# Kernel optimization log

Hardware: AMD Instinct MI355X
Metric: run time of the kernel (lower is better)

## Reference

```python
import jax, jax.numpy as jnp
import numpy as np

B, I, H = 16384, 1024, 1024
W_SCALE = 0.03  # keep gate pre-activations in a sane range (mimics small init)


def setup_inputs() -> dict:
    key = jax.random.key(0)
    ks = jax.random.split(key, 7)
    return {
        "x": jax.random.normal(ks[0], (B, I), dtype=jnp.float32),
        "c": jax.random.normal(ks[1], (B, H), dtype=jnp.float32),
        "h": jax.random.normal(ks[2], (B, H), dtype=jnp.float32),
        # gate order along axis 0: f (forget), i (input), k (cell cand), o (output)
        "Wx": jax.random.normal(ks[3], (4, H, I), dtype=jnp.float32) * W_SCALE,
        "bx": jax.random.normal(ks[4], (4, H), dtype=jnp.float32) * W_SCALE,
        "Wh": jax.random.normal(ks[5], (4, H, H), dtype=jnp.float32) * W_SCALE,
        "bh": jax.random.normal(ks[6], (4, H), dtype=jnp.float32) * W_SCALE,
    }


def reference(x, c, h, Wx, bx, Wh, bh):
    # Fused equivalent of the 8 tiny nn.Linear calls: one stacked GEMM each
    # for input->hidden and hidden->hidden. pre: [B, 4, H]
    pre = (jnp.einsum('bi,ghi->bgh', x, Wx)
           + jnp.einsum('bk,ghk->bgh', h, Wh)
           + bx[None] + bh[None])
    f = jax.nn.sigmoid(pre[:, 0])   # forget gate (w1/r1)
    i = jax.nn.sigmoid(pre[:, 1])   # input gate  (w2/r2)
    k = jnp.tanh(pre[:, 2])         # cell candidate (w3/r3)
    o = jax.nn.sigmoid(pre[:, 3])   # output gate (w4/r4)
    c_new = f * c + i * k
    h_new = o * jnp.tanh(c_new)
    return (o, c_new, h_new)
```

## Files before the change

### kernel.cpp

```cpp
#include <hip/hip_runtime.h>
#include <hip/hip_bf16.h>
#include <cstdint>

#define DI __device__ __forceinline__

typedef __attribute__((ext_vector_type(4))) float f32x4;
typedef __attribute__((ext_vector_type(8))) short bf16x8;

static constexpr int B_ = 16384, I_ = 1024, H_ = 1024;
static constexpr int M = B_;
static constexpr int N = 4 * H_;
static constexpr int K = I_ + H_;
static constexpr int NT = K / 64;

static constexpr size_t OFF_A  = 0;
static constexpr size_t OFF_W  = OFF_A + (size_t)M * K * 2;
static constexpr size_t OFF_BI = OFF_W + (size_t)N * K * 2;
static constexpr size_t OFF_G  = OFF_BI + (size_t)N * 4;

DI unsigned short f2bf(float f) {
    union { float f; unsigned u; } v; v.f = f;
    unsigned r = v.u + 0x7FFFu + ((v.u >> 16) & 1u);
    return (unsigned short)(r >> 16);
}
DI float bf2f(unsigned short u) {
    union { unsigned u; float f; } v; v.u = ((unsigned)u) << 16; return v.f;
}

__global__ void cvt_kernel(const float* __restrict__ x, const float* __restrict__ h,
                           const float* __restrict__ Wx, const float* __restrict__ Wh,
                           unsigned short* __restrict__ A, unsigned short* __restrict__ W)
{
    long tid = (long)blockIdx.x * blockDim.x + threadIdx.x;
    long row = tid >> 9;
    int  col = (int)(tid & 511) * 4;
    const float* src;
    unsigned short* dst;
    if (row < M) {
        src = (col < I_) ? x + (size_t)row * I_ + col
                         : h + (size_t)row * H_ + (col - I_);
        dst = A + (size_t)row * K + col;
    } else {
        long r = row - M;
        src = (col < I_) ? Wx + (size_t)r * I_ + col
                         : Wh + (size_t)r * H_ + (col - I_);
        dst = W + (size_t)r * K + col;
    }
    float4 v = *(const float4*)src;
    ushort4 o;
    o.x = f2bf(v.x); o.y = f2bf(v.y); o.z = f2bf(v.z); o.w = f2bf(v.w);
    *(ushort4*)dst = o;
}

__global__ void bias_kernel(const float* __restrict__ bx, const float* __restrict__ bh,
                            float* __restrict__ bias)
{
    int i = blockIdx.x * blockDim.x + threadIdx.x;
    if (i < N) bias[i] = bx[i] + bh[i];
}

DI void stage_half(const unsigned short* __restrict__ g, int grow0, int kcol,
                   unsigned short* ldsbase, int tid)
{
    const int w    = tid >> 6, lane = tid & 63;
    const int rsub = (w << 3) + (lane >> 3);
    const int kk   = kcol + (((lane & 7) ^ (lane >> 3)) << 3);
#pragma unroll
    for (int l = 0; l < 2; ++l) {
        const unsigned short* gp = g + (size_t)(grow0 + (l << 6) + rsub) * K + kk;
        unsigned short* lp = ldsbase + (((l << 6) + (w << 3)) << 6);
        __builtin_amdgcn_global_load_lds(
            (const __attribute__((address_space(1))) void*)gp,
            (__attribute__((address_space(3))) void*)lp, 16, 0, 0);
    }
}

DI bf16x8 ldfrag(const unsigned short* tile, int row, int ks, int lane)
{
    const int sl = ((ks << 2) + (lane >> 4)) ^ (lane & 7);
    return *(const bf16x8*)(tile + (row << 6) + (sl << 3));
}

DI void fbar() {
    __builtin_amdgcn_sched_barrier(0);
    __builtin_amdgcn_s_barrier();
    __builtin_amdgcn_sched_barrier(0);
}

#define MFMA_QUAD(MH, N0)                                                     \
  _Pragma("unroll") for (int m_ = 0; m_ < 4; ++m_)                            \
  _Pragma("unroll") for (int dn_ = 0; dn_ < 2; ++dn_)                         \
  _Pragma("unroll") for (int ks_ = 0; ks_ < 2; ++ks_)                         \
    acc[(MH)*4 + m_][(N0) + dn_] = __builtin_amdgcn_mfma_f32_16x16x32_bf16(   \
        a[m_][ks_], b[(N0) + dn_][ks_], acc[(MH)*4 + m_][(N0) + dn_], 0, 0, 0);

__global__ __launch_bounds__(512, 2) void gemm_gates(
    const unsigned short* __restrict__ Abf, const unsigned short* __restrict__ Wbf,
    const float* __restrict__ bias, __hip_bfloat16* __restrict__ G)
{
    __shared__ __align__(16) unsigned short sh[65536];

    const int tid  = threadIdx.x;
    const int lane = tid & 63;
    const int wid  = tid >> 6;
    const int wr   = wid >> 2;
    const int wc   = wid & 3;

    const int bid  = blockIdx.x;
    const int wg   = ((bid & 7) << 7) | (bid >> 3);
    const int nbk  = wg & 15, mbk = wg >> 4;
    const int brow = mbk << 8, bcol = nbk << 8;

    const int l15  = lane & 15;
    const int rA0  = (wr << 7) + l15;
    const int rB0  = (wc << 6) + l15;

    f32x4 acc[8][4];
#pragma unroll
    for (int i = 0; i < 8; ++i)
#pragma unroll
        for (int j = 0; j < 4; ++j) acc[i][j] = f32x4{0.f, 0.f, 0.f, 0.f};
    bf16x8 a[4][2], b[4][2];

    {
        unsigned short* A0 = sh;
        unsigned short* B0 = sh + 16384;
        unsigned short* A1 = sh + 32768;
        stage_half(Abf, brow,       0, A0,        tid);
        stage_half(Abf, brow + 128, 0, A0 + 8192, tid);
        stage_half(Wbf, bcol,       0, B0,        tid);
        stage_half(Wbf, bcol + 128, 0, B0 + 8192, tid);
        stage_half(Abf, brow,      64, A1,        tid);
        asm volatile("s_waitcnt vmcnt(2)" ::: "memory");
        fbar();
    }

    for (int t = 0; t < NT; ++t) {
        const int q = t & 1;
        unsigned short* curA = sh + q * 32768;
        unsigned short* curB = curA + 16384;
        unsigned short* nxtA = sh + (q ^ 1) * 32768;
        unsigned short* nxtB = nxtA + 16384;
        const int k1 = (t + 1) << 6, k2 = (t + 2) << 6;

#pragma unroll
        for (int m = 0; m < 4; ++m)
#pragma unroll
            for (int ks = 0; ks < 2; ++ks)
                a[m][ks] = ldfrag(curA, rA0 + m * 16, ks, lane);
#pragma unroll
        for (int n = 0; n < 2; ++n)
#pragma unroll
            for (int ks = 0; ks < 2; ++ks)
                b[n][ks] = ldfrag(curB, rB0 + n * 16, ks, lane);
        if (t + 1 < NT) stage_half(Abf, brow + 128, k1, nxtA + 8192, tid);
        fbar();
        __builtin_amdgcn_s_setprio(1);
        MFMA_QUAD(0, 0);
        __builtin_amdgcn_s_setprio(0);
        fbar();

#pragma unroll
        for (int n = 2; n < 4; ++n)
#pragma unroll
            for (int ks = 0; ks < 2; ++ks)
                b[n][ks] = ldfrag(curB, rB0 + n * 16, ks, lane);
        if (t + 1 < NT) stage_half(Wbf, bcol, k1, nxtB, tid);
        fbar();
        __builtin_amdgcn_s_setprio(1);
        MFMA_QUAD(0, 2);
        __builtin_amdgcn_s_setprio(0);
        fbar();

#pragma unroll
        for (int m = 0; m < 4; ++m)
#pragma unroll
            for (int ks = 0; ks < 2; ++ks)
                a[m][ks] = ldfrag(curA, rA0 + 64 + m * 16, ks, lane);
        if (t + 1 < NT) stage_half(Wbf, bcol + 128, k1, nxtB + 8192, tid);
        fbar();
        __builtin_amdgcn_s_setprio(1);
        MFMA_QUAD(1, 2);
        __builtin_amdgcn_s_setprio(0);
        fbar();

        if (t + 2 < NT) {
            stage_half(Abf, brow, k2, curA, tid);
            asm volatile("s_waitcnt vmcnt(2)" ::: "memory");
        } else {
            asm volatile("s_waitcnt vmcnt(0)" ::: "memory");
        }
        fbar();
        __builtin_amdgcn_s_setprio(1);
        MFMA_QUAD(1, 0);
        __builtin_amdgcn_s_setprio(0);
        fbar();
    }

    const int gate  = bcol >> 10;
    const int crow0 = brow + (wr << 7) + ((lane >> 4) << 2);
    const int ccol0 = bcol + (wc << 6) + l15;
#pragma unroll
    for (int n = 0; n < 4; ++n) {
        const int col = ccol0 + n * 16;
        const float bs = bias[col];
#pragma unroll
        for (int mf = 0; mf < 8; ++mf) {
#pragma unroll
            for (int j = 0; j < 4; ++j) {
                float v = acc[mf][n][j] + bs;
                float r;
                if (gate == 2) {
                    float vc = fminf(fmaxf(v, -15.f), 15.f);
                    float e  = __expf(2.f * vc);
                    r = (e - 1.f) / (e + 1.f);
                } else {
                    r = 1.f / (1.f + __expf(-v));
                }
                G[(size_t)(crow0 + mf * 16 + j) * N + col] = __float2bfloat16(r);
            }
        }
    }
}

__global__ void lstm_elem(const unsigned short* __restrict__ G,
                          const float* __restrict__ c, float* __restrict__ out)
{
    long tid = (long)blockIdx.x * blockDim.x + threadIdx.x;
    long bq  = tid >> 8;
    int  hc  = (int)(tid & 255) * 4;
    const unsigned short* g0 = G + (size_t)bq * N;

    ushort4 fu = *(const ushort4*)(g0 + hc);
    ushort4 iu = *(const ushort4*)(g0 + 1024 + hc);
    ushort4 ku = *(const ushort4*)(g0 + 2048 + hc);
    ushort4 ou = *(const ushort4*)(g0 + 3072 + hc);
    float4  cv = *(const float4*)(c + (size_t)bq * H_ + hc);

    float fv[4] = {bf2f(fu.x), bf2f(fu.y), bf2f(fu.z), bf2f(fu.w)};
    float iv[4] = {bf2f(iu.x), bf2f(iu.y), bf2f(iu.z), bf2f(iu.w)};
    float kv[4] = {bf2f(ku.x), bf2f(ku.y), bf2f(ku.z), bf2f(ku.w)};
    float ov[4] = {bf2f(ou.x), bf2f(ou.y), bf2f(ou.z), bf2f(ou.w)};
    float cc[4] = {cv.x, cv.y, cv.z, cv.w};

    float4 o4, cn4, hn4;
    float* o4p = (float*)&o4; float* cn4p = (float*)&cn4; float* hn4p = (float*)&hn4;
#pragma unroll
    for (int j = 0; j < 4; ++j) {
        float cn = fv[j] * cc[j] + iv[j] * kv[j];
        o4p[j]  = ov[j];
        cn4p[j] = cn;
        hn4p[j] = ov[j] * tanhf(cn);
    }
    const size_t base = (size_t)bq * H_ + hc;
    const size_t P = (size_t)B_ * H_;
    *(float4*)(out + base)         = o4;
    *(float4*)(out + P + base)     = cn4;
    *(float4*)(out + 2 * P + base) = hn4;
}

extern "C" void kernel_launch(void* const* d_in, const int* in_sizes, int n_in,
                              void* d_out, int out_size, void* d_ws, size_t ws_size,
                              hipStream_t stream)
{
    const float* x  = (const float*)d_in[0];
    const float* c  = (const float*)d_in[1];
    const float* h  = (const float*)d_in[2];
    const float* Wx = (const float*)d_in[3];
    const float* bx = (const float*)d_in[4];
    const float* Wh = (const float*)d_in[5];
    const float* bh = (const float*)d_in[6];

    unsigned short* Abf  = (unsigned short*)((char*)d_ws + OFF_A);
    unsigned short* Wbf  = (unsigned short*)((char*)d_ws + OFF_W);
    float*          bias = (float*)((char*)d_ws + OFF_BI);
    unsigned short* G    = (unsigned short*)((char*)d_ws + OFF_G);
    float*          out  = (float*)d_out;

    cvt_kernel<<<40960, 256, 0, stream>>>(x, h, Wx, Wh, Abf, Wbf);
    bias_kernel<<<16, 256, 0, stream>>>(bx, bh, bias);
    gemm_gates<<<(M / 256) * (N / 256), 512, 0, stream>>>(
        Abf, Wbf, bias, (__hip_bfloat16*)G);
    lstm_elem<<<(B_ * H_ / 4) / 256, 256, 0, stream>>>(G, c, out);
}
```

Before: 393.2 us.

## Interleave gate weight rows and fuse LSTM cell update into GEMM epilogue

Weight and bias rows are permuted during conversion so that each 16-column group in a GEMM tile holds the f, i, k and o gates for the same hidden units. This lets the GEMM epilogue compute all four gates, read c, and write o, c_new and h_new directly. The separate elementwise kernel and the bf16 gate buffer round trip go away. In exchange, epilogue stores are scalar 4-byte writes with 16-lane contiguity instead of float4, and the epilogue does more work per thread.

Result: faster. 332.7 us (-15.4%).

```diff
diff --git a/kernel.cpp b/kernel.cpp
--- a/kernel.cpp
+++ b/kernel.cpp
@@ -16,15 +16,11 @@
 static constexpr size_t OFF_A  = 0;
 static constexpr size_t OFF_W  = OFF_A + (size_t)M * K * 2;
 static constexpr size_t OFF_BI = OFF_W + (size_t)N * K * 2;
-static constexpr size_t OFF_G  = OFF_BI + (size_t)N * 4;
 
 DI unsigned short f2bf(float f) {
     union { float f; unsigned u; } v; v.f = f;
     unsigned r = v.u + 0x7FFFu + ((v.u >> 16) & 1u);
     return (unsigned short)(r >> 16);
-}
-DI float bf2f(unsigned short u) {
-    union { unsigned u; float f; } v; v.u = ((unsigned)u) << 16; return v.f;
 }
 
 __global__ void cvt_kernel(const float* __restrict__ x, const float* __restrict__ h,
@@ -41,9 +37,12 @@
                          : h + (size_t)row * H_ + (col - I_);
         dst = A + (size_t)row * K + col;
     } else {
-        long r = row - M;
-        src = (col < I_) ? Wx + (size_t)r * I_ + col
-                         : Wh + (size_t)r * H_ + (col - I_);
+        int r = (int)(row - M);
+        int gate = (r >> 4) & 3;
+        int hcol = ((r >> 6) << 4) | (r & 15);
+        int srow = gate * H_ + hcol;
+        src = (col < I_) ? Wx + (size_t)srow * I_ + col
+                         : Wh + (size_t)srow * H_ + (col - I_);
         dst = W + (size_t)r * K + col;
     }
     float4 v = *(const float4*)src;
@@ -55,8 +54,13 @@
 __global__ void bias_kernel(const float* __restrict__ bx, const float* __restrict__ bh,
                             float* __restrict__ bias)
 {
-    int i = blockIdx.x * blockDim.x + threadIdx.x;
-    if (i < N) bias[i] = bx[i] + bh[i];
+    int r = blockIdx.x * blockDim.x + threadIdx.x;
+    if (r < N) {
+        int gate = (r >> 4) & 3;
+        int hcol = ((r >> 6) << 4) | (r & 15);
+        int s = gate * H_ + hcol;
+        bias[r] = bx[s] + bh[s];
+    }
 }
 
 DI void stage_half(const unsigned short* __restrict__ g, int grow0, int kcol,
@@ -87,6 +91,13 @@
     __builtin_amdgcn_sched_barrier(0);
 }
 
+DI float sigf(float v) { return 1.f / (1.f + __expf(-v)); }
+DI float tanhfast(float v) {
+    float vc = fminf(fmaxf(v, -15.f), 15.f);
+    float e  = __expf(2.f * vc);
+    return (e - 1.f) / (e + 1.f);
+}
+
 #define MFMA_QUAD(MH, N0)                                                     \
   _Pragma("unroll") for (int m_ = 0; m_ < 4; ++m_)                            \
   _Pragma("unroll") for (int dn_ = 0; dn_ < 2; ++dn_)                         \
@@ -94,9 +105,10 @@
     acc[(MH)*4 + m_][(N0) + dn_] = __builtin_amdgcn_mfma_f32_16x16x32_bf16(   \
         a[m_][ks_], b[(N0) + dn_][ks_], acc[(MH)*4 + m_][(N0) + dn_], 0, 0, 0);
 
-__global__ __launch_bounds__(512, 2) void gemm_gates(
+__global__ __launch_bounds__(512, 2) void gemm_lstm(
     const unsigned short* __restrict__ Abf, const unsigned short* __restrict__ Wbf,
-    const float* __restrict__ bias, __hip_bfloat16* __restrict__ G)
+    const float* __restrict__ bias, const float* __restrict__ c,
+    float* __restrict__ out)
 {
     __shared__ __align__(16) unsigned short sh[65536];
 
@@ -197,66 +209,32 @@
         fbar();
     }
 
-    const int gate  = bcol >> 10;
+    const int hcol  = (((nbk << 2) + wc) << 4) + l15;
     const int crow0 = brow + (wr << 7) + ((lane >> 4) << 2);
-    const int ccol0 = bcol + (wc << 6) + l15;
-#pragma unroll
-    for (int n = 0; n < 4; ++n) {
-        const int col = ccol0 + n * 16;
-        const float bs = bias[col];
-#pragma unroll
-        for (int mf = 0; mf < 8; ++mf) {
-#pragma unroll
-            for (int j = 0; j < 4; ++j) {
-                float v = acc[mf][n][j] + bs;
-                float r;
-                if (gate == 2) {
-                    float vc = fminf(fmaxf(v, -15.f), 15.f);
-                    float e  = __expf(2.f * vc);
-                    r = (e - 1.f) / (e + 1.f);
-                } else {
-                    r = 1.f / (1.f + __expf(-v));
-                }
-                G[(size_t)(crow0 + mf * 16 + j) * N + col] = __float2bfloat16(r);
-            }
+    const int cb0   = bcol + (wc << 6) + l15;
+    const float bs0 = bias[cb0];
+    const float bs1 = bias[cb0 + 16];
+    const float bs2 = bias[cb0 + 32];
+    const float bs3 = bias[cb0 + 48];
+    const size_t P  = (size_t)B_ * H_;
+#pragma unroll
+    for (int mf = 0; mf < 8; ++mf) {
+#pragma unroll
+        for (int j = 0; j < 4; ++j) {
+            const int row = crow0 + mf * 16 + j;
+            const size_t base = (size_t)row * H_ + hcol;
+            float fg = sigf(acc[mf][0][j] + bs0);
+            float ig = sigf(acc[mf][1][j] + bs1);
+            float kg = tanhfast(acc[mf][2][j] + bs2);
+            float og = sigf(acc[mf][3][j] + bs3);
+            float cv = c[base];
+            float cn = fg * cv + ig * kg;
+            float hn = og * tanhfast(cn);
+            out[base]         = og;
+            out[P + base]     = cn;
+            out[2 * P + base] = hn;
         }
     }
-}
-
-__global__ void lstm_elem(const unsigned short* __restrict__ G,
-                          const float* __restrict__ c, float* __restrict__ out)
-{
-    long tid = (long)blockIdx.x * blockDim.x + threadIdx.x;
-    long bq  = tid >> 8;
-    int  hc  = (int)(tid & 255) * 4;
-    const unsigned short* g0 = G + (size_t)bq * N;
-
-    ushort4 fu = *(const ushort4*)(g0 + hc);
-    ushort4 iu = *(const ushort4*)(g0 + 1024 + hc);
-    ushort4 ku = *(const ushort4*)(g0 + 2048 + hc);
-    ushort4 ou = *(const ushort4*)(g0 + 3072 + hc);
-    float4  cv = *(const float4*)(c + (size_t)bq * H_ + hc);
-
-    float fv[4] = {bf2f(fu.x), bf2f(fu.y), bf2f(fu.z), bf2f(fu.w)};
-    float iv[4] = {bf2f(iu.x), bf2f(iu.y), bf2f(iu.z), bf2f(iu.w)};
-    float kv[4] = {bf2f(ku.x), bf2f(ku.y), bf2f(ku.z), bf2f(ku.w)};
-    float ov[4] = {bf2f(ou.x), bf2f(ou.y), bf2f(ou.z), bf2f(ou.w)};
-    float cc[4] = {cv.x, cv.y, cv.z, cv.w};
-
-    float4 o4, cn4, hn4;
-    float* o4p = (float*)&o4; float* cn4p = (float*)&cn4; float* hn4p = (float*)&hn4;
-#pragma unroll
-    for (int j = 0; j < 4; ++j) {
-        float cn = fv[j] * cc[j] + iv[j] * kv[j];
-        o4p[j]  = ov[j];
-        cn4p[j] = cn;
-        hn4p[j] = ov[j] * tanhf(cn);
-    }
-    const size_t base = (size_t)bq * H_ + hc;
-    const size_t P = (size_t)B_ * H_;
-    *(float4*)(out + base)         = o4;
-    *(float4*)(out + P + base)     = cn4;
-    *(float4*)(out + 2 * P + base) = hn4;
 }
 
 extern "C" void kernel_launch(void* const* d_in, const int* in_sizes, int n_in,
@@ -274,12 +252,10 @@
     unsigned short* Abf  = (unsigned short*)((char*)d_ws + OFF_A);
     unsigned short* Wbf  = (unsigned short*)((char*)d_ws + OFF_W);
     float*          bias = (float*)((char*)d_ws + OFF_BI);
-    unsigned short* G    = (unsigned short*)((char*)d_ws + OFF_G);
     float*          out  = (float*)d_out;
 
     cvt_kernel<<<40960, 256, 0, stream>>>(x, h, Wx, Wh, Abf, Wbf);
     bias_kernel<<<16, 256, 0, stream>>>(bx, bh, bias);
-    gemm_gates<<<(M / 256) * (N / 256), 512, 0, stream>>>(
-        Abf, Wbf, bias, (__hip_bfloat16*)G);
-    lstm_elem<<<(B_ * H_ / 4) / 256, 256, 0, stream>>>(G, c, out);
-}
+    gemm_lstm<<<(M / 256) * (N / 256), 512, 0, stream>>>(
+        Abf, Wbf, bias, c, out);
+}
```
